# Optimization experiments

Measured on AMD Instinct MI355X. Metric: run time of the kernel, lower is better.

## Reference

```python
import jax, jax.numpy as jnp
import numpy as np

DIM = 2048
NUM_HEADS = 16
HEAD_DIM = DIM // NUM_HEADS
BATCH, SEQ = 2, 2048


def setup_inputs() -> dict:
    key = jax.random.key(0)
    kx, kq, kk, kv, ko = jax.random.split(key, 5)
    scale = 1.0 / np.sqrt(DIM)
    return {
        "x": jax.random.normal(kx, (BATCH, SEQ, DIM), dtype=jnp.float32),
        "Wq": jax.random.normal(kq, (DIM, DIM), dtype=jnp.float32) * scale,
        "Wk": jax.random.normal(kk, (DIM, DIM), dtype=jnp.float32) * scale,
        "Wv": jax.random.normal(kv, (DIM, DIM), dtype=jnp.float32) * scale,
        "Wo": jax.random.normal(ko, (DIM, DIM), dtype=jnp.float32) * scale,
    }


def reference(x, Wq, Wk, Wv, Wo):
    b, s, _ = x.shape
    # QKV projections (flax Dense, no bias): y = x @ W
    q = (x @ Wq).reshape(b, s, NUM_HEADS, HEAD_DIM)
    k = (x @ Wk).reshape(b, s, NUM_HEADS, HEAD_DIM)
    v = (x @ Wv).reshape(b, s, NUM_HEADS, HEAD_DIM)
    # full (non-causal) softmax attention, scores are [b, h, q, k]
    scores = jnp.einsum('bqhd,bkhd->bhqk', q, k) * (HEAD_DIM ** -0.5)
    attn = jax.nn.softmax(scores, axis=-1)
    out = jnp.einsum('bhqk,bkhd->bqhd', attn, v).reshape(b, s, DIM)
    return out @ Wo
```

## Files before the change

### kernel.cpp

```cpp
#include <hip/hip_runtime.h>
#include <stdint.h>


typedef unsigned short u16;
typedef __attribute__((ext_vector_type(8))) short bf16x8;
typedef __attribute__((ext_vector_type(4))) float f32x4;
typedef __attribute__((ext_vector_type(2))) unsigned int u32x2;

__device__ __forceinline__ u16 f2bf(float f) {
  union { float f; uint32_t u; } v; v.f = f;
  return (u16)((v.u + 0x7fffu + ((v.u >> 16) & 1u)) >> 16);
}

__device__ __forceinline__ float fast_exp2(float x) {
#if __has_builtin(__builtin_amdgcn_exp2f)
  return __builtin_amdgcn_exp2f(x);
#else
  return exp2f(x);
#endif
}

__device__ __forceinline__ void gl_lds16(const void* g, void* l) {
  __builtin_amdgcn_global_load_lds(
      (const __attribute__((address_space(1))) unsigned int*)g,
      (__attribute__((address_space(3))) unsigned int*)l, 16, 0, 0);
}

__global__ __launch_bounds__(256) void sniff_k(const u16* __restrict__ x,
                                               int* __restrict__ flag) {
  __shared__ int cnt;
  const int t = threadIdx.x;
  if (t == 0) cnt = 0;
  __syncthreads();
  int sane = 0;
#pragma unroll
  for (int i = 0; i < 16; ++i) {
    u16 u = x[t * 16 + i];
    int e = (u >> 7) & 0xff;
    sane += (e >= 90 && e <= 150) ? 1 : 0;
  }
  atomicAdd(&cnt, sane);
  __syncthreads();
  if (t == 0) *flag = (cnt >= 3700) ? 0 : 1;
}

__global__ __launch_bounds__(256) void convert_x_k(const void* __restrict__ xin,
                                                   u16* __restrict__ xb,
                                                   const int* __restrict__ flag) {
  if (*flag == 0) return;
  const int i = (blockIdx.x * 256 + threadIdx.x) * 8;
  const float* xf = (const float*)xin;
  float4 a = *(const float4*)(xf + i);
  float4 b = *(const float4*)(xf + i + 4);
  bf16x8 o;
  o[0] = (short)f2bf(a.x); o[1] = (short)f2bf(a.y);
  o[2] = (short)f2bf(a.z); o[3] = (short)f2bf(a.w);
  o[4] = (short)f2bf(b.x); o[5] = (short)f2bf(b.y);
  o[6] = (short)f2bf(b.z); o[7] = (short)f2bf(b.w);
  *(bf16x8*)(xb + i) = o;
}

__global__ __launch_bounds__(256) void convert_transpose_k(const void* __restrict__ w0,
                                                           const void* __restrict__ w1,
                                                           const void* __restrict__ w2,
                                                           const void* __restrict__ w3,
                                                           u16* __restrict__ out_base,
                                                           const int* __restrict__ flag) {
  __shared__ u16 tile[64][66];
  const int z = blockIdx.z;
  const void* in = (z == 0) ? w0 : (z == 1) ? w1 : (z == 2) ? w2 : w3;
  u16* out = out_base + (size_t)z * 4194304u;
  const int tr = blockIdx.y, tc = blockIdx.x, t = threadIdx.x;
  if (*flag) {
    const float* inf32 = (const float*)in;
#pragma unroll
    for (int i = 0; i < 16; ++i) {
      int idx = t + i * 256, r = idx >> 6, c = idx & 63;
      tile[r][c] = f2bf(inf32[(size_t)(tr * 64 + r) * 2048 + tc * 64 + c]);
    }
  } else {
    const u16* inb = (const u16*)in;
#pragma unroll
    for (int i = 0; i < 16; ++i) {
      int idx = t + i * 256, r = idx >> 6, c = idx & 63;
      tile[r][c] = inb[(size_t)(tr * 64 + r) * 2048 + tc * 64 + c];
    }
  }
  __syncthreads();
#pragma unroll
  for (int i = 0; i < 16; ++i) {
    int idx = t + i * 256, r = idx >> 6, c = idx & 63;
    out[(size_t)(tc * 64 + r) * 2048 + tr * 64 + c] = tile[c][r];
  }
}

__global__ __launch_bounds__(256) void transpose_k(const u16* __restrict__ in,
                                                   u16* __restrict__ out) {
  __shared__ u16 tile[64][66];
  const size_t zoff = (size_t)blockIdx.z * 4194304u;
  in += zoff; out += zoff;
  const int tr = blockIdx.y, tc = blockIdx.x, t = threadIdx.x;
#pragma unroll
  for (int i = 0; i < 16; ++i) {
    int idx = t + i * 256, r = idx >> 6, c = idx & 63;
    tile[r][c] = in[(size_t)(tr * 64 + r) * 2048 + tc * 64 + c];
  }
  __syncthreads();
#pragma unroll
  for (int i = 0; i < 16; ++i) {
    int idx = t + i * 256, r = idx >> 6, c = idx & 63;
    out[(size_t)(tc * 64 + r) * 2048 + tr * 64 + c] = tile[c][r];
  }
}

__global__ __launch_bounds__(256) void gemm_bt(const u16* __restrict__ A,
                                               const void* __restrict__ Araw,
                                               const int* __restrict__ aflag,
                                               const u16* __restrict__ Bt,
                                               u16* __restrict__ C0,
                                               u16* __restrict__ C1,
                                               u16* __restrict__ C2,
                                               float qscale,
                                               const int* __restrict__ outflag) {
  __shared__ u16 As[128 * 64];
  __shared__ u16 Bs[128 * 64];
  const int bx = blockIdx.x, by = blockIdx.y, t = threadIdx.x;
  const int wave = t >> 6, lane = t & 63;
  const int g = lane >> 4, lq = lane & 15;
  const int wr = wave >> 1, wc = wave & 1;
  const int which = bx >> 4, nb = bx & 15;
  u16* C = (which == 0) ? C0 : ((which == 1) ? C1 : C2);
  const float scale = (which == 0) ? qscale : 1.0f;
  const u16* Ause = (aflag && *aflag == 0) ? (const u16*)Araw : A;
  const int lr = lane >> 3, lcs = ((lane & 7) ^ lr) * 8;

  const u16* Arow = Ause + (size_t)(by * 128) * 2048;
  const u16* Brow = Bt + (size_t)(bx * 128) * 2048;

  int cofs[2];
#pragma unroll
  for (int ks = 0; ks < 2; ++ks) cofs[ks] = ((ks * 4 + g) ^ (lq & 7)) * 8;

  f32x4 acc[4][4];
#pragma unroll
  for (int i = 0; i < 4; ++i)
#pragma unroll
    for (int j = 0; j < 4; ++j) acc[i][j] = f32x4{0.f, 0.f, 0.f, 0.f};

  for (int kb = 0; kb < 2048; kb += 64) {
    __syncthreads();
#pragma unroll
    for (int i = 0; i < 4; ++i) {
      const int r = wave * 32 + i * 8;
      gl_lds16(Arow + (size_t)(r + lr) * 2048 + kb + lcs, &As[r * 64]);
      gl_lds16(Brow + (size_t)(r + lr) * 2048 + kb + lcs, &Bs[r * 64]);
    }
    __syncthreads();
#pragma unroll
    for (int ks = 0; ks < 2; ++ks) {
      bf16x8 af[4], bfr[4];
#pragma unroll
      for (int mt = 0; mt < 4; ++mt)
        af[mt] = *(const bf16x8*)(&As[(wr * 64 + mt * 16 + lq) * 64 + cofs[ks]]);
#pragma unroll
      for (int nt = 0; nt < 4; ++nt)
        bfr[nt] = *(const bf16x8*)(&Bs[(wc * 64 + nt * 16 + lq) * 64 + cofs[ks]]);
#pragma unroll
      for (int mt = 0; mt < 4; ++mt)
#pragma unroll
        for (int nt = 0; nt < 4; ++nt)
          acc[mt][nt] = __builtin_amdgcn_mfma_f32_16x16x32_bf16(af[mt], bfr[nt], acc[mt][nt], 0, 0, 0);
    }
  }
  const int outF32 = outflag ? *outflag : 0;
#pragma unroll
  for (int mt = 0; mt < 4; ++mt)
#pragma unroll
    for (int nt = 0; nt < 4; ++nt)
#pragma unroll
      for (int j = 0; j < 4; ++j) {
        size_t row = (size_t)(by * 128 + wr * 64 + mt * 16 + g * 4 + j);
        size_t col = (size_t)(nb * 128 + wc * 64 + nt * 16 + lq);
        float v = acc[mt][nt][j] * scale;
        if (outF32) ((float*)C)[row * 2048 + col] = v;
        else C[row * 2048 + col] = f2bf(v);
      }
}

__global__ __launch_bounds__(256, 4) void attn_kernel(const u16* __restrict__ Q,
                                                      const u16* __restrict__ K,
                                                      const u16* __restrict__ Vt,
                                                      u16* __restrict__ O) {
  __shared__ u16 Ks[64 * 128];
  __shared__ u16 Vs[128 * 64];

  const int qb = blockIdx.x, h = blockIdx.y, b = blockIdx.z;
  const int t = threadIdx.x, wave = t >> 6, lane = t & 63;
  const int g = lane >> 4, lq = lane & 15;

  const size_t qk_base = ((size_t)b * 2048) * 2048 + (size_t)h * 128;
  const size_t vt_base = ((size_t)b * 2048 + (size_t)h * 128) * 2048;

  bf16x8 qf[4];
  {
    const u16* qp = Q + qk_base + (size_t)(qb * 64 + wave * 16 + lq) * 2048 + g * 8;
#pragma unroll
    for (int kk = 0; kk < 4; ++kk) qf[kk] = *(const bf16x8*)(qp + kk * 32);
  }

  f32x4 acc_o[8];
#pragma unroll
  for (int i = 0; i < 8; ++i) acc_o[i] = f32x4{0.f, 0.f, 0.f, 0.f};
  float l_run = 0.f;

  const int vlr = lane >> 3, vlcs = ((lane & 7) ^ vlr) * 8;

  int kofs[4];
#pragma unroll
  for (int kk = 0; kk < 4; ++kk) kofs[kk] = ((kk * 4 + g) ^ (lq & 7)) * 8;

  for (int kb = 0; kb < 2048; kb += 64) {
    __syncthreads();
#pragma unroll
    for (int i = 0; i < 4; ++i) {
      const int win = wave * 2 + (i >> 1), half = i & 1;
      const int kr = half * 4 + (lane >> 4);
      const int kc = (lane & 15) ^ kr;
      gl_lds16(K + qk_base + (size_t)(kb + win * 8 + kr) * 2048 + kc * 8,
               &Ks[win * 1024 + half * 512]);
      const int vr = wave * 32 + i * 8;
      gl_lds16(Vt + vt_base + (size_t)(vr + vlr) * 2048 + kb + vlcs,
               &Vs[vr * 64]);
    }
    __syncthreads();

    f32x4 st[4];
#pragma unroll
    for (int mt = 0; mt < 4; ++mt) st[mt] = f32x4{0.f, 0.f, 0.f, 0.f};
#pragma unroll
    for (int kk = 0; kk < 4; ++kk)
#pragma unroll
      for (int mt = 0; mt < 4; ++mt) {
        bf16x8 af = *(const bf16x8*)(&Ks[(mt * 16 + lq) * 128 + kofs[kk]]);
        st[mt] = __builtin_amdgcn_mfma_f32_16x16x32_bf16(af, qf[kk], st[mt], 0, 0, 0);
      }

    uint32_t c[4][2];
#pragma unroll
    for (int mt = 0; mt < 4; ++mt) {
      float p0 = fast_exp2(st[mt][0]);
      float p1 = fast_exp2(st[mt][1]);
      float p2 = fast_exp2(st[mt][2]);
      float p3 = fast_exp2(st[mt][3]);
      l_run += (p0 + p1) + (p2 + p3);
      asm("v_cvt_pk_bf16_f32 %0, %1, %2" : "=v"(c[mt][0]) : "v"(p0), "v"(p1));
      asm("v_cvt_pk_bf16_f32 %0, %1, %2" : "=v"(c[mt][1]) : "v"(p2), "v"(p3));
    }

#pragma unroll
    for (int kk = 0; kk < 2; ++kk) {
      u32x2 s0 = __builtin_amdgcn_permlane32_swap(c[2 * kk][0], c[2 * kk + 1][0], false, false);
      u32x2 r0 = __builtin_amdgcn_permlane16_swap(s0[0], s0[1], false, false);
      u32x2 s1 = __builtin_amdgcn_permlane32_swap(c[2 * kk][1], c[2 * kk + 1][1], false, false);
      u32x2 r1 = __builtin_amdgcn_permlane16_swap(s1[0], s1[1], false, false);
      union { uint32_t d[4]; bf16x8 v; } af;
      af.d[0] = r0[0];
      af.d[1] = r1[0];
      af.d[2] = r0[1];
      af.d[3] = r1[1];
#pragma unroll
      for (int nt = 0; nt < 8; ++nt) {
        bf16x8 bfr = *(const bf16x8*)(&Vs[(nt * 16 + lq) * 64 + ((kk * 4 + g) ^ (lq & 7)) * 8]);
        acc_o[nt] = __builtin_amdgcn_mfma_f32_16x16x32_bf16(af.v, bfr, acc_o[nt], 0, 0, 0);
      }
    }
  }

  l_run += __shfl_xor(l_run, 16);
  l_run += __shfl_xor(l_run, 32);
  const float i0 = 1.f / __shfl(l_run, g * 4 + 0);
  const float i1 = 1.f / __shfl(l_run, g * 4 + 1);
  const float i2 = 1.f / __shfl(l_run, g * 4 + 2);
  const float i3 = 1.f / __shfl(l_run, g * 4 + 3);
  u16* op = O + ((size_t)b * 2048 + qb * 64 + wave * 16) * 2048 + h * 128;
#pragma unroll
  for (int nt = 0; nt < 8; ++nt) {
    op[(size_t)(g * 4 + 0) * 2048 + nt * 16 + lq] = f2bf(acc_o[nt][0] * i0);
    op[(size_t)(g * 4 + 1) * 2048 + nt * 16 + lq] = f2bf(acc_o[nt][1] * i1);
    op[(size_t)(g * 4 + 2) * 2048 + nt * 16 + lq] = f2bf(acc_o[nt][2] * i2);
    op[(size_t)(g * 4 + 3) * 2048 + nt * 16 + lq] = f2bf(acc_o[nt][3] * i3);
  }
}

extern "C" void kernel_launch(void* const* d_in, const int* in_sizes, int n_in,
                              void* d_out, int out_size, void* d_ws, size_t ws_size,
                              hipStream_t stream) {
  const void* x  = d_in[0];
  const void* Wq = d_in[1];
  const void* Wk = d_in[2];
  const void* Wv = d_in[3];
  const void* Wo = d_in[4];
  u16* ws = (u16*)d_ws;

  const size_t SLOT = 4194304u;
  u16* xb  = ws + 0 * SLOT;
  u16* WqT = ws + 2 * SLOT;
  u16* WoT = ws + 5 * SLOT;
  u16* Qb  = ws + 6 * SLOT;
  u16* Kb  = ws + 8 * SLOT;
  u16* Vb  = ws + 10 * SLOT;
  int* flag = (int*)(ws + 12 * SLOT);
  u16* VTd = (u16*)d_out;
  u16* Ab  = Qb;

  sniff_k<<<1, 256, 0, stream>>>((const u16*)x, flag);

  convert_x_k<<<4096, 256, 0, stream>>>(x, xb, flag);
  convert_transpose_k<<<dim3(32, 32, 4), 256, 0, stream>>>(Wq, Wk, Wv, Wo, WqT, flag);

  const float QSCALE = 0.12751745f;
  gemm_bt<<<dim3(48, 32), 256, 0, stream>>>(xb, x, flag, WqT, Qb, Kb, Vb,
                                            QSCALE, nullptr);

  transpose_k<<<dim3(32, 32, 2), 256, 0, stream>>>(Vb, VTd);

  attn_kernel<<<dim3(32, 16, 2), dim3(256), 0, stream>>>(Qb, Kb, VTd, Ab);

  gemm_bt<<<dim3(16, 32), 256, 0, stream>>>(Ab, Ab, nullptr, WoT,
                                            (u16*)d_out, (u16*)d_out, (u16*)d_out,
                                            1.0f, flag);
}
```

Before: 409.3 us.

## Replace QKV projection GEMM with 256x256-tile double-buffered 512-thread kernel

Adds a new gemm256 kernel for the fused QKV projection. It uses 256x256 output tiles, 8 waves, double-buffered direct global-to-LDS loads with an XOR swizzle, and interleaves LDS fragment reads with MFMA blocks under raised wave priority. It also remaps block IDs for L2 locality. The larger tile is meant to raise arithmetic intensity and hide load latency. In exchange it uses much more register and LDS space per block, which lowers occupancy, and its output stores are scattered 16-bit writes.

New measurement: 416.7 us. Within noise of the previous version (+1.8%).

```diff
diff --git a/kernel.cpp b/kernel.cpp
--- a/kernel.cpp
+++ b/kernel.cpp
@@ -111,6 +111,140 @@
     int idx = t + i * 256, r = idx >> 6, c = idx & 63;
     out[(size_t)(tc * 64 + r) * 2048 + tr * 64 + c] = tile[c][r];
   }
+}
+
+__global__ __launch_bounds__(512, 2) void gemm256(const u16* __restrict__ A,
+                                                  const void* __restrict__ Araw,
+                                                  const int* __restrict__ aflag,
+                                                  const u16* __restrict__ Bt,
+                                                  u16* __restrict__ Cbase,
+                                                  float qscale) {
+  __shared__ __align__(16) u16 Ls[2][2][256 * 64];
+
+  const int t = threadIdx.x, wave = t >> 6, lane = t & 63;
+  const int g = lane >> 4, lq = lane & 15;
+  const int wr = wave >> 2, wc = wave & 3;
+  const int bid = blockIdx.x;
+  const int swz = (bid & 7) * 48 + (bid >> 3);
+  const int bm = swz / 24, bn = swz % 24;
+
+  const u16* Ause = (*aflag == 0) ? (const u16*)Araw : A;
+  const u16* Arow = Ause + (size_t)(bm * 256) * 2048;
+  const u16* Brow = Bt + (size_t)(bn * 256) * 2048;
+  const int lr = lane >> 3, lcs = ((lane & 7) ^ lr) * 8;
+
+  int cofs[2];
+#pragma unroll
+  for (int kk = 0; kk < 2; ++kk) cofs[kk] = ((kk * 4 + g) ^ (lq & 7)) * 8;
+
+  f32x4 acc[8][4];
+#pragma unroll
+  for (int i = 0; i < 8; ++i)
+#pragma unroll
+    for (int j = 0; j < 4; ++j) acc[i][j] = f32x4{0.f, 0.f, 0.f, 0.f};
+
+  auto stage = [&](int tt) {
+    u16* Al = &Ls[tt & 1][0][0];
+    u16* Bl = &Ls[tt & 1][1][0];
+    const int kb = tt * 64;
+#pragma unroll
+    for (int i = 0; i < 4; ++i) {
+      const int s = wave * 4 + i;
+      gl_lds16(Arow + (size_t)(s * 8 + lr) * 2048 + kb + lcs, Al + s * 8 * 64);
+      gl_lds16(Brow + (size_t)(s * 8 + lr) * 2048 + kb + lcs, Bl + s * 8 * 64);
+    }
+  };
+
+  stage(0);
+  stage(1);
+
+  for (int kt = 0; kt < 32; ++kt) {
+    if (kt < 31) asm volatile("s_waitcnt vmcnt(8)" ::: "memory");
+    else         asm volatile("s_waitcnt vmcnt(0)" ::: "memory");
+    __builtin_amdgcn_sched_barrier(0);
+    __builtin_amdgcn_s_barrier();
+
+    const u16* Al = &Ls[kt & 1][0][0];
+    const u16* Bl = &Ls[kt & 1][1][0];
+
+    bf16x8 af[8], bf0[4], bf1[4];
+#pragma unroll
+    for (int m = 0; m < 4; ++m)
+#pragma unroll
+      for (int kk = 0; kk < 2; ++kk)
+        af[m * 2 + kk] = *(const bf16x8*)(&Al[(wr * 128 + m * 16 + lq) * 64 + cofs[kk]]);
+#pragma unroll
+    for (int n = 0; n < 2; ++n)
+#pragma unroll
+      for (int kk = 0; kk < 2; ++kk)
+        bf0[n * 2 + kk] = *(const bf16x8*)(&Bl[(wc * 64 + n * 16 + lq) * 64 + cofs[kk]]);
+    __builtin_amdgcn_s_setprio(1);
+#pragma unroll
+    for (int m = 0; m < 4; ++m)
+#pragma unroll
+      for (int n = 0; n < 2; ++n)
+#pragma unroll
+        for (int kk = 0; kk < 2; ++kk)
+          acc[m][n] = __builtin_amdgcn_mfma_f32_16x16x32_bf16(af[m * 2 + kk], bf0[n * 2 + kk], acc[m][n], 0, 0, 0);
+    __builtin_amdgcn_s_setprio(0);
+#pragma unroll
+    for (int n = 0; n < 2; ++n)
+#pragma unroll
+      for (int kk = 0; kk < 2; ++kk)
+        bf1[n * 2 + kk] = *(const bf16x8*)(&Bl[(wc * 64 + (2 + n) * 16 + lq) * 64 + cofs[kk]]);
+    __builtin_amdgcn_s_setprio(1);
+#pragma unroll
+    for (int m = 0; m < 4; ++m)
+#pragma unroll
+      for (int n = 0; n < 2; ++n)
+#pragma unroll
+        for (int kk = 0; kk < 2; ++kk)
+          acc[m][2 + n] = __builtin_amdgcn_mfma_f32_16x16x32_bf16(af[m * 2 + kk], bf1[n * 2 + kk], acc[m][2 + n], 0, 0, 0);
+    __builtin_amdgcn_s_setprio(0);
+#pragma unroll
+    for (int m = 0; m < 4; ++m)
+#pragma unroll
+      for (int kk = 0; kk < 2; ++kk)
+        af[m * 2 + kk] = *(const bf16x8*)(&Al[(wr * 128 + (4 + m) * 16 + lq) * 64 + cofs[kk]]);
+    __builtin_amdgcn_s_setprio(1);
+#pragma unroll
+    for (int m = 0; m < 4; ++m)
+#pragma unroll
+      for (int n = 0; n < 2; ++n)
+#pragma unroll
+        for (int kk = 0; kk < 2; ++kk)
+          acc[4 + m][2 + n] = __builtin_amdgcn_mfma_f32_16x16x32_bf16(af[m * 2 + kk], bf1[n * 2 + kk], acc[4 + m][2 + n], 0, 0, 0);
+    __builtin_amdgcn_s_setprio(0);
+    __builtin_amdgcn_s_setprio(1);
+#pragma unroll
+    for (int m = 0; m < 4; ++m)
+#pragma unroll
+      for (int n = 0; n < 2; ++n)
+#pragma unroll
+        for (int kk = 0; kk < 2; ++kk)
+          acc[4 + m][n] = __builtin_amdgcn_mfma_f32_16x16x32_bf16(af[m * 2 + kk], bf0[n * 2 + kk], acc[4 + m][n], 0, 0, 0);
+    __builtin_amdgcn_s_setprio(0);
+
+    asm volatile("s_waitcnt lgkmcnt(0)" ::: "memory");
+    __builtin_amdgcn_sched_barrier(0);
+    __builtin_amdgcn_s_barrier();
+    if (kt < 30) stage(kt + 2);
+  }
+
+  const int which = bn >> 3;
+  u16* C = Cbase + (size_t)which * 2u * 4194304u;
+  const float scale = (which == 0) ? qscale : 1.0f;
+  const int colbase = (bn & 7) * 256 + wc * 64;
+#pragma unroll
+  for (int m = 0; m < 8; ++m)
+#pragma unroll
+    for (int n = 0; n < 4; ++n)
+#pragma unroll
+      for (int j = 0; j < 4; ++j) {
+        size_t row = (size_t)(bm * 256 + wr * 128 + m * 16 + g * 4 + j);
+        size_t col = (size_t)(colbase + n * 16 + lq);
+        C[row * 2048 + col] = f2bf(acc[m][n][j] * scale);
+      }
 }
 
 __global__ __launch_bounds__(256) void gemm_bt(const u16* __restrict__ A,
@@ -319,8 +453,7 @@
   convert_transpose_k<<<dim3(32, 32, 4), 256, 0, stream>>>(Wq, Wk, Wv, Wo, WqT, flag);
 
   const float QSCALE = 0.12751745f;
-  gemm_bt<<<dim3(48, 32), 256, 0, stream>>>(xb, x, flag, WqT, Qb, Kb, Vb,
-                                            QSCALE, nullptr);
+  gemm256<<<384, 512, 0, stream>>>(xb, x, flag, WqT, Qb, QSCALE);
 
   transpose_k<<<dim3(32, 32, 2), 256, 0, stream>>>(Vb, VTd);
 
```
